# Kernel tuning notes

Hardware: AMD Instinct MI355X
Metric: run time of the kernel (lower is better)

## Reference

```python
import jax, jax.numpy as jnp
import numpy as np

B, T, C = 4, 4096, 1024
DIM_K, DIM_V = 64, 64


def setup_inputs() -> dict:
    key = jax.random.key(0)
    k1, k2, k3, k4, k5, k6 = jax.random.split(key, 6)
    q_embs = jax.random.normal(k1, (B, T, C), dtype=jnp.float32)
    k_embs = jax.random.normal(k2, (B, T, C), dtype=jnp.float32)
    v_embs = jax.random.normal(k3, (B, T, C), dtype=jnp.float32)
    # nn.Linear(C, dim) weights have shape (dim, C); y = x @ W.T
    s = 1.0 / np.sqrt(C)
    w_q = jax.random.uniform(k4, (DIM_K, C), jnp.float32, -s, s)
    w_k = jax.random.uniform(k5, (DIM_K, C), jnp.float32, -s, s)
    w_v = jax.random.uniform(k6, (DIM_V, C), jnp.float32, -s, s)
    return {"q_embs": q_embs, "k_embs": k_embs, "v_embs": v_embs,
            "w_q": w_q, "w_k": w_k, "w_v": w_v}


def reference(q_embs, k_embs, v_embs, w_q, w_k, w_v):
    Bv, Tv, Cv = v_embs.shape
    q = jnp.einsum('btc,kc->btk', q_embs, w_q)  # [B,T,dim_k]
    k = jnp.einsum('btc,kc->btk', k_embs, w_k)  # [B,T,dim_k]
    v = jnp.einsum('btc,vc->btv', v_embs, w_v)  # [B,T,dim_v]
    # NOTE: original scales by C**-0.5 (embedding dim), not dim_k**-0.5
    scores = jnp.einsum('bqk,bsk->bqs', q, k) * (Cv ** -0.5)  # [B,T,T]
    causal = jnp.tril(jnp.ones((Tv, Tv), dtype=bool))
    scores = jnp.where(causal, scores, -jnp.inf)
    wei = jax.nn.softmax(scores, axis=-1)
    return jnp.einsum('bqs,bsv->bqv', wei, v)  # [B,T,dim_v]
```

## Files before the change

### kernel.cpp

```cpp
#include <hip/hip_runtime.h>

#define TSEQ 4096
#define CDIM 1024
#define DHEAD 64

typedef __bf16 bf16x8 __attribute__((ext_vector_type(8)));
typedef float f32x4 __attribute__((ext_vector_type(4)));

__global__ __launch_bounds__(256) void wconv_kernel(
    const float* __restrict__ wq, const float* __restrict__ wk,
    const float* __restrict__ wv, __bf16* __restrict__ Wb)
{
  const int t = blockIdx.x * 256 + threadIdx.x;
  const int idx = t * 8;
  const int pid = idx >> 16;
  const float* __restrict__ src = (pid == 0) ? wq : ((pid == 1) ? wk : wv);
  const int off = idx & 65535;
  f32x4 a = *(const f32x4*)(src + off);
  f32x4 b = *(const f32x4*)(src + off + 4);
  ushort4 lo, hi;
  lo.x = __builtin_bit_cast(unsigned short, (__bf16)a[0]);
  lo.y = __builtin_bit_cast(unsigned short, (__bf16)a[1]);
  lo.z = __builtin_bit_cast(unsigned short, (__bf16)a[2]);
  lo.w = __builtin_bit_cast(unsigned short, (__bf16)a[3]);
  hi.x = __builtin_bit_cast(unsigned short, (__bf16)b[0]);
  hi.y = __builtin_bit_cast(unsigned short, (__bf16)b[1]);
  hi.z = __builtin_bit_cast(unsigned short, (__bf16)b[2]);
  hi.w = __builtin_bit_cast(unsigned short, (__bf16)b[3]);
  *(ushort4*)(Wb + idx) = lo;
  *(ushort4*)(Wb + idx + 4) = hi;
}

#define PKCH 64
#define PNCH (CDIM / PKCH)

__global__ __launch_bounds__(256) void proj_kernel(
    const float* __restrict__ qe, const float* __restrict__ ke,
    const float* __restrict__ ve, const __bf16* __restrict__ Wb,
    __bf16* __restrict__ Qo, __bf16* __restrict__ Ko, __bf16* __restrict__ Vto)
{
  __shared__ __align__(16) float Abuf[2][64 * PKCH];

  const int pid = blockIdx.y;
  const float* __restrict__ emb = (pid == 0) ? qe : ((pid == 1) ? ke : ve);
  const __bf16* __restrict__ W = Wb + (size_t)pid * DHEAD * CDIM;

  const int wave = threadIdx.x >> 6;
  const int lane = threadIdx.x & 63;
  const int g = lane >> 4, c = lane & 15;
  const int bm0 = blockIdx.x * 64;
  const int m0 = bm0 + wave * 16;

  size_t gsrc[4];
  int lofs[4];
#pragma unroll
  for (int j = 0; j < 4; ++j) {
    const int row = (wave * 4 + j) * 4 + (lane >> 4);
    const int colb = ((lane & 15) << 4) ^ ((row & 7) << 4);
    gsrc[j] = (size_t)(bm0 + row) * CDIM + (colb >> 2);
    lofs[j] = (wave * 4 + j) * 256;
  }

  const int arow = wave * 16 + c;
  const int aswz = (arow & 7) << 4;
  int ra0[2], ra1[2];
#pragma unroll
  for (int ks = 0; ks < 2; ++ks) {
    const int ncol = ks * 128 + g * 32;
    ra0[ks] = arow * 256 + ((ncol) ^ aswz);
    ra1[ks] = arow * 256 + ((ncol + 16) ^ aswz);
  }

  f32x4 acc[4];
#pragma unroll
  for (int n = 0; n < 4; ++n) acc[n] = (f32x4){0.f, 0.f, 0.f, 0.f};

  auto stage = [&](int buf, int ch) {
    const float* __restrict__ eb = emb + (size_t)ch * PKCH;
    float* lb = &Abuf[buf][0];
#pragma unroll
    for (int j = 0; j < 4; ++j) {
      __builtin_amdgcn_global_load_lds(
          (const __attribute__((address_space(1))) void*)(uintptr_t)(eb + gsrc[j]),
          (__attribute__((address_space(3))) void*)(unsigned)(uintptr_t)(lb + lofs[j]),
          16, 0, 0);
    }
  };

  stage(0, 0);
  __syncthreads();

  for (int ch = 0; ch < PNCH; ++ch) {
    if (ch + 1 < PNCH) stage((ch + 1) & 1, ch + 1);
    const char* base = (const char*)&Abuf[ch & 1][0];
    const __bf16* __restrict__ wp = W + (size_t)ch * PKCH + g * 8;
#pragma unroll
    for (int ks = 0; ks < 2; ++ks) {
      f32x4 lo = *(const f32x4*)(base + ra0[ks]);
      f32x4 hi = *(const f32x4*)(base + ra1[ks]);
      bf16x8 af;
      af[0] = (__bf16)lo[0];
      af[1] = (__bf16)lo[1];
      af[2] = (__bf16)lo[2];
      af[3] = (__bf16)lo[3];
      af[4] = (__bf16)hi[0];
      af[5] = (__bf16)hi[1];
      af[6] = (__bf16)hi[2];
      af[7] = (__bf16)hi[3];
#pragma unroll
      for (int n = 0; n < 4; ++n) {
        bf16x8 wf = *(const bf16x8*)(wp + (size_t)(n * 16 + c) * CDIM + ks * 32);
        acc[n] = __builtin_amdgcn_mfma_f32_16x16x32_bf16(af, wf, acc[n], 0, 0, 0);
      }
    }
    __syncthreads();
  }

  if (pid < 2) {
    __bf16* __restrict__ dst = (pid == 0) ? Qo : Ko;
#pragma unroll
    for (int n = 0; n < 4; ++n)
#pragma unroll
      for (int r = 0; r < 4; ++r)
        dst[(size_t)(m0 + g * 4 + r) * DHEAD + n * 16 + c] = (__bf16)acc[n][r];
  } else {
    const int t0 = m0 + g * 4;
    const int bb = t0 >> 12;
    const int tl = t0 & (TSEQ - 1);
#pragma unroll
    for (int n = 0; n < 4; ++n) {
      const int v = n * 16 + c;
      ushort4 pk;
      pk.x = __builtin_bit_cast(unsigned short, (__bf16)acc[n][0]);
      pk.y = __builtin_bit_cast(unsigned short, (__bf16)acc[n][1]);
      pk.z = __builtin_bit_cast(unsigned short, (__bf16)acc[n][2]);
      pk.w = __builtin_bit_cast(unsigned short, (__bf16)acc[n][3]);
      *(ushort4*)(Vto + ((size_t)bb * DHEAD + v) * TSEQ + tl) = pk;
    }
  }
}

#define NWAVE 8

__global__ __launch_bounds__(512) void attn_kernel(
    const __bf16* __restrict__ Q, const __bf16* __restrict__ K,
    const __bf16* __restrict__ Vt, float* __restrict__ out)
{
  __shared__ __bf16 Plds[NWAVE][16][72];
  __shared__ float Om[NWAVE][16][65];
  __shared__ float La[NWAVE][16];

  const int b = blockIdx.y;
  const int tile = (int)gridDim.x - 1 - (int)blockIdx.x;
  const int q0 = tile * 16;
  const int wave = threadIdx.x >> 6;
  const int lane = threadIdx.x & 63;
  const int g = lane >> 4, c = lane & 15;

  const __bf16* Qb = Q + (size_t)b * TSEQ * DHEAD;
  const __bf16* Kb = K + (size_t)b * TSEQ * DHEAD;
  const __bf16* Vb = Vt + (size_t)b * DHEAD * TSEQ;

  bf16x8 aq0 = *(const bf16x8*)(Qb + (size_t)(q0 + c) * DHEAD + g * 8);
  bf16x8 aq1 = *(const bf16x8*)(Qb + (size_t)(q0 + c) * DHEAD + 32 + g * 8);

  bf16x8 ones;
#pragma unroll
  for (int j = 0; j < 8; ++j) ones[j] = (__bf16)1.0f;

  f32x4 o[4];
#pragma unroll
  for (int n = 0; n < 4; ++n) o[n] = (f32x4){0.f, 0.f, 0.f, 0.f};
  f32x4 lacc = (f32x4){0.f, 0.f, 0.f, 0.f};

  const float kScale = 0.04508422f;
  const int nt = (q0 + 16 + 63) >> 6;

  for (int st = wave; st < nt; st += 2 * NWAVE) {
    const int s0A = st * 64;
    const int stB = st + NWAVE;
    const bool hasB = stB < nt;
    const int s0B = stB * 64;

    bf16x8 ka0[4], ka1[4], kb0[4], kb1[4];
#pragma unroll
    for (int n = 0; n < 4; ++n) {
      const __bf16* kp = Kb + (size_t)(s0A + n * 16 + c) * DHEAD + g * 8;
      ka0[n] = *(const bf16x8*)(kp);
      ka1[n] = *(const bf16x8*)(kp + 32);
    }
    if (hasB) {
#pragma unroll
      for (int n = 0; n < 4; ++n) {
        const __bf16* kp = Kb + (size_t)(s0B + n * 16 + c) * DHEAD + g * 8;
        kb0[n] = *(const bf16x8*)(kp);
        kb1[n] = *(const bf16x8*)(kp + 32);
      }
    }

    f32x4 sA[4];
#pragma unroll
    for (int n = 0; n < 4; ++n) {
      f32x4 z = (f32x4){0.f, 0.f, 0.f, 0.f};
      z = __builtin_amdgcn_mfma_f32_16x16x32_bf16(aq0, ka0[n], z, 0, 0, 0);
      sA[n] = __builtin_amdgcn_mfma_f32_16x16x32_bf16(aq1, ka1[n], z, 0, 0, 0);
    }
    bf16x8 va0[4], va1[4];
#pragma unroll
    for (int n = 0; n < 4; ++n) {
      const __bf16* vp = Vb + (size_t)(n * 16 + c) * TSEQ + s0A + g * 8;
      va0[n] = *(const bf16x8*)(vp);
      va1[n] = *(const bf16x8*)(vp + 32);
    }
#pragma unroll
    for (int n = 0; n < 4; ++n) {
      const int sidx = s0A + n * 16 + c;
#pragma unroll
      for (int r = 0; r < 4; ++r) {
        const int qidx = q0 + g * 4 + r;
        float p = (sidx <= qidx) ? __builtin_amdgcn_exp2f(sA[n][r] * kScale) : 0.f;
        Plds[wave][g * 4 + r][n * 16 + c] = (__bf16)p;
      }
    }

    f32x4 sB[4];
    bf16x8 vb0[4], vb1[4];
    if (hasB) {
#pragma unroll
      for (int n = 0; n < 4; ++n) {
        f32x4 z = (f32x4){0.f, 0.f, 0.f, 0.f};
        z = __builtin_amdgcn_mfma_f32_16x16x32_bf16(aq0, kb0[n], z, 0, 0, 0);
        sB[n] = __builtin_amdgcn_mfma_f32_16x16x32_bf16(aq1, kb1[n], z, 0, 0, 0);
      }
#pragma unroll
      for (int n = 0; n < 4; ++n) {
        const __bf16* vp = Vb + (size_t)(n * 16 + c) * TSEQ + s0B + g * 8;
        vb0[n] = *(const bf16x8*)(vp);
        vb1[n] = *(const bf16x8*)(vp + 32);
      }
    }

    bf16x8 p0A = *(const bf16x8*)(&Plds[wave][c][g * 8]);
    bf16x8 p1A = *(const bf16x8*)(&Plds[wave][c][32 + g * 8]);
    lacc = __builtin_amdgcn_mfma_f32_16x16x32_bf16(p0A, ones, lacc, 0, 0, 0);
    lacc = __builtin_amdgcn_mfma_f32_16x16x32_bf16(p1A, ones, lacc, 0, 0, 0);

    if (hasB) {
#pragma unroll
      for (int n = 0; n < 4; ++n) {
        const int sidx = s0B + n * 16 + c;
#pragma unroll
        for (int r = 0; r < 4; ++r) {
          const int qidx = q0 + g * 4 + r;
          float p = (sidx <= qidx) ? __builtin_amdgcn_exp2f(sB[n][r] * kScale) : 0.f;
          Plds[wave][g * 4 + r][n * 16 + c] = (__bf16)p;
        }
      }
    }

#pragma unroll
    for (int n = 0; n < 4; ++n) {
      o[n] = __builtin_amdgcn_mfma_f32_16x16x32_bf16(p0A, va0[n], o[n], 0, 0, 0);
      o[n] = __builtin_amdgcn_mfma_f32_16x16x32_bf16(p1A, va1[n], o[n], 0, 0, 0);
    }

    if (hasB) {
      bf16x8 p0B = *(const bf16x8*)(&Plds[wave][c][g * 8]);
      bf16x8 p1B = *(const bf16x8*)(&Plds[wave][c][32 + g * 8]);
      lacc = __builtin_amdgcn_mfma_f32_16x16x32_bf16(p0B, ones, lacc, 0, 0, 0);
      lacc = __builtin_amdgcn_mfma_f32_16x16x32_bf16(p1B, ones, lacc, 0, 0, 0);
#pragma unroll
      for (int n = 0; n < 4; ++n) {
        o[n] = __builtin_amdgcn_mfma_f32_16x16x32_bf16(p0B, vb0[n], o[n], 0, 0, 0);
        o[n] = __builtin_amdgcn_mfma_f32_16x16x32_bf16(p1B, vb1[n], o[n], 0, 0, 0);
      }
    }
  }

#pragma unroll
  for (int n = 0; n < 4; ++n)
#pragma unroll
    for (int r = 0; r < 4; ++r)
      Om[wave][g * 4 + r][n * 16 + c] = o[n][r];
  if (c == 0) {
#pragma unroll
    for (int r = 0; r < 4; ++r) La[wave][g * 4 + r] = lacc[r];
  }
  __syncthreads();

  const int tid = threadIdx.x;
  const int q = tid >> 5;
  const int c2 = (tid & 31) * 2;
  float l = 0.f;
#pragma unroll
  for (int w = 0; w < NWAVE; ++w) l += La[w][q];
  float s0 = 0.f, s1 = 0.f;
#pragma unroll
  for (int w = 0; w < NWAVE; ++w) {
    s0 += Om[w][q][c2];
    s1 += Om[w][q][c2 + 1];
  }
  const float inv = 1.0f / l;
  float2 r;
  r.x = s0 * inv;
  r.y = s1 * inv;
  *(float2*)(out + ((size_t)b * TSEQ + q0 + q) * DHEAD + c2) = r;
}

extern "C" void kernel_launch(void* const* d_in, const int* in_sizes, int n_in,
                              void* d_out, int out_size, void* d_ws, size_t ws_size,
                              hipStream_t stream) {
  const float* qe = (const float*)d_in[0];
  const float* ke = (const float*)d_in[1];
  const float* ve = (const float*)d_in[2];
  const float* wq = (const float*)d_in[3];
  const float* wk = (const float*)d_in[4];
  const float* wv = (const float*)d_in[5];

  __bf16* Qw  = (__bf16*)d_ws;
  __bf16* Kw  = Qw + (size_t)4 * TSEQ * DHEAD;
  __bf16* Vtw = Kw + (size_t)4 * TSEQ * DHEAD;
  __bf16* Wb  = Vtw + (size_t)4 * TSEQ * DHEAD;

  wconv_kernel<<<dim3(96), dim3(256), 0, stream>>>(wq, wk, wv, Wb);

  dim3 g1(4 * TSEQ / 64, 3), b1(256);
  proj_kernel<<<g1, b1, 0, stream>>>(qe, ke, ve, Wb, Qw, Kw, Vtw);

  dim3 g2(TSEQ / 16, 4), b2(512);
  attn_kernel<<<g2, b2, 0, stream>>>(Qw, Kw, Vtw, (float*)d_out);
}
```

Measured before the change: 279.8 us.

## Split projection K dimension across waves with 16-row blocks and LDS reduction

The projection kernel now gives each block 16 rows instead of 64. It loads each row's full 1024-float embedding into LDS in one shot rather than double-buffering 64-wide chunks. Each of the four waves covers a quarter of the K dimension, and the partial accumulators are summed through LDS before vectorized bf16 stores of Q/K and transposed V. The grid grows fourfold to raise memory-level parallelism on this bandwidth-bound stage. In exchange, each block uses 64KB of LDS, which limits blocks per CU, adds a cross-wave reduction, and drops the load/compute pipelining.

```diff
diff --git a/kernel.cpp b/kernel.cpp
--- a/kernel.cpp
+++ b/kernel.cpp
@@ -31,112 +31,102 @@
   *(ushort4*)(Wb + idx + 4) = hi;
 }
 
-#define PKCH 64
-#define PNCH (CDIM / PKCH)
-
 __global__ __launch_bounds__(256) void proj_kernel(
     const float* __restrict__ qe, const float* __restrict__ ke,
     const float* __restrict__ ve, const __bf16* __restrict__ Wb,
     __bf16* __restrict__ Qo, __bf16* __restrict__ Ko, __bf16* __restrict__ Vto)
 {
-  __shared__ __align__(16) float Abuf[2][64 * PKCH];
+  __shared__ __align__(16) float Alds[16 * 1024];
 
   const int pid = blockIdx.y;
   const float* __restrict__ emb = (pid == 0) ? qe : ((pid == 1) ? ke : ve);
   const __bf16* __restrict__ W = Wb + (size_t)pid * DHEAD * CDIM;
 
-  const int wave = threadIdx.x >> 6;
+  const int wav = threadIdx.x >> 6;
   const int lane = threadIdx.x & 63;
   const int g = lane >> 4, c = lane & 15;
-  const int bm0 = blockIdx.x * 64;
-  const int m0 = bm0 + wave * 16;
-
-  size_t gsrc[4];
-  int lofs[4];
-#pragma unroll
-  for (int j = 0; j < 4; ++j) {
-    const int row = (wave * 4 + j) * 4 + (lane >> 4);
-    const int colb = ((lane & 15) << 4) ^ ((row & 7) << 4);
-    gsrc[j] = (size_t)(bm0 + row) * CDIM + (colb >> 2);
-    lofs[j] = (wave * 4 + j) * 256;
-  }
-
-  const int arow = wave * 16 + c;
-  const int aswz = (arow & 7) << 4;
-  int ra0[2], ra1[2];
-#pragma unroll
-  for (int ks = 0; ks < 2; ++ks) {
-    const int ncol = ks * 128 + g * 32;
-    ra0[ks] = arow * 256 + ((ncol) ^ aswz);
-    ra1[ks] = arow * 256 + ((ncol + 16) ^ aswz);
-  }
+  const int m0 = blockIdx.x * 16;
+
+#pragma unroll
+  for (int r = 0; r < 16; ++r) {
+    const float* src = emb + (size_t)(m0 + r) * CDIM + wav * 256 + ((lane ^ (r & 7)) << 2);
+    float* dst = Alds + r * 1024 + wav * 256;
+    __builtin_amdgcn_global_load_lds(
+        (const __attribute__((address_space(1))) void*)(uintptr_t)src,
+        (__attribute__((address_space(3))) void*)(unsigned)(uintptr_t)dst,
+        16, 0, 0);
+  }
+  asm volatile("s_waitcnt vmcnt(0)" ::: "memory");
 
   f32x4 acc[4];
 #pragma unroll
   for (int n = 0; n < 4; ++n) acc[n] = (f32x4){0.f, 0.f, 0.f, 0.f};
 
-  auto stage = [&](int buf, int ch) {
-    const float* __restrict__ eb = emb + (size_t)ch * PKCH;
-    float* lb = &Abuf[buf][0];
-#pragma unroll
-    for (int j = 0; j < 4; ++j) {
-      __builtin_amdgcn_global_load_lds(
-          (const __attribute__((address_space(1))) void*)(uintptr_t)(eb + gsrc[j]),
-          (__attribute__((address_space(3))) void*)(unsigned)(uintptr_t)(lb + lofs[j]),
-          16, 0, 0);
-    }
-  };
-
-  stage(0, 0);
+  const int cswz = c & 7;
+  const __bf16* __restrict__ wbase = W + (size_t)c * CDIM + wav * 256 + g * 8;
+#pragma unroll
+  for (int ks = 0; ks < 8; ++ks) {
+    const float* ab = Alds + c * 1024 + wav * 256 + ks * 32;
+    f32x4 lo = *(const f32x4*)(ab + (((g * 2 + 0) ^ cswz) << 2));
+    f32x4 hi = *(const f32x4*)(ab + (((g * 2 + 1) ^ cswz) << 2));
+    bf16x8 af;
+    af[0] = (__bf16)lo[0];
+    af[1] = (__bf16)lo[1];
+    af[2] = (__bf16)lo[2];
+    af[3] = (__bf16)lo[3];
+    af[4] = (__bf16)hi[0];
+    af[5] = (__bf16)hi[1];
+    af[6] = (__bf16)hi[2];
+    af[7] = (__bf16)hi[3];
+#pragma unroll
+    for (int n = 0; n < 4; ++n) {
+      bf16x8 wf = *(const bf16x8*)(wbase + (size_t)n * 16 * CDIM + ks * 32);
+      acc[n] = __builtin_amdgcn_mfma_f32_16x16x32_bf16(af, wf, acc[n], 0, 0, 0);
+    }
+  }
+
   __syncthreads();
-
-  for (int ch = 0; ch < PNCH; ++ch) {
-    if (ch + 1 < PNCH) stage((ch + 1) & 1, ch + 1);
-    const char* base = (const char*)&Abuf[ch & 1][0];
-    const __bf16* __restrict__ wp = W + (size_t)ch * PKCH + g * 8;
-#pragma unroll
-    for (int ks = 0; ks < 2; ++ks) {
-      f32x4 lo = *(const f32x4*)(base + ra0[ks]);
-      f32x4 hi = *(const f32x4*)(base + ra1[ks]);
-      bf16x8 af;
-      af[0] = (__bf16)lo[0];
-      af[1] = (__bf16)lo[1];
-      af[2] = (__bf16)lo[2];
-      af[3] = (__bf16)lo[3];
-      af[4] = (__bf16)hi[0];
-      af[5] = (__bf16)hi[1];
-      af[6] = (__bf16)hi[2];
-      af[7] = (__bf16)hi[3];
-#pragma unroll
-      for (int n = 0; n < 4; ++n) {
-        bf16x8 wf = *(const bf16x8*)(wp + (size_t)(n * 16 + c) * CDIM + ks * 32);
-        acc[n] = __builtin_amdgcn_mfma_f32_16x16x32_bf16(af, wf, acc[n], 0, 0, 0);
-      }
-    }
-    __syncthreads();
-  }
-
+  float* Ored = Alds;
+#pragma unroll
+  for (int n = 0; n < 4; ++n)
+#pragma unroll
+    for (int r = 0; r < 4; ++r)
+      Ored[wav * 1152 + (g * 4 + r) * 72 + n * 16 + c] = acc[n][r];
+  __syncthreads();
+
+  const int t = threadIdx.x;
   if (pid < 2) {
     __bf16* __restrict__ dst = (pid == 0) ? Qo : Ko;
-#pragma unroll
-    for (int n = 0; n < 4; ++n)
-#pragma unroll
-      for (int r = 0; r < 4; ++r)
-        dst[(size_t)(m0 + g * 4 + r) * DHEAD + n * 16 + c] = (__bf16)acc[n][r];
+    const int row = t >> 4, c4 = (t & 15) * 4;
+    f32x4 s = (f32x4){0.f, 0.f, 0.f, 0.f};
+#pragma unroll
+    for (int w2 = 0; w2 < 4; ++w2) {
+      f32x4 p = *(const f32x4*)&Ored[w2 * 1152 + row * 72 + c4];
+      s[0] += p[0]; s[1] += p[1]; s[2] += p[2]; s[3] += p[3];
+    }
+    ushort4 pk;
+    pk.x = __builtin_bit_cast(unsigned short, (__bf16)s[0]);
+    pk.y = __builtin_bit_cast(unsigned short, (__bf16)s[1]);
+    pk.z = __builtin_bit_cast(unsigned short, (__bf16)s[2]);
+    pk.w = __builtin_bit_cast(unsigned short, (__bf16)s[3]);
+    *(ushort4*)(dst + (size_t)(m0 + row) * DHEAD + c4) = pk;
   } else {
-    const int t0 = m0 + g * 4;
-    const int bb = t0 >> 12;
-    const int tl = t0 & (TSEQ - 1);
-#pragma unroll
-    for (int n = 0; n < 4; ++n) {
-      const int v = n * 16 + c;
-      ushort4 pk;
-      pk.x = __builtin_bit_cast(unsigned short, (__bf16)acc[n][0]);
-      pk.y = __builtin_bit_cast(unsigned short, (__bf16)acc[n][1]);
-      pk.z = __builtin_bit_cast(unsigned short, (__bf16)acc[n][2]);
-      pk.w = __builtin_bit_cast(unsigned short, (__bf16)acc[n][3]);
-      *(ushort4*)(Vto + ((size_t)bb * DHEAD + v) * TSEQ + tl) = pk;
-    }
+    const int v = t >> 2, tq = (t & 3) * 4;
+    const int bb = m0 >> 12;
+    const int tl = m0 & (TSEQ - 1);
+    float s[4];
+#pragma unroll
+    for (int j = 0; j < 4; ++j) {
+      s[j] = 0.f;
+#pragma unroll
+      for (int w2 = 0; w2 < 4; ++w2) s[j] += Ored[w2 * 1152 + (tq + j) * 72 + v];
+    }
+    ushort4 pk;
+    pk.x = __builtin_bit_cast(unsigned short, (__bf16)s[0]);
+    pk.y = __builtin_bit_cast(unsigned short, (__bf16)s[1]);
+    pk.z = __builtin_bit_cast(unsigned short, (__bf16)s[2]);
+    pk.w = __builtin_bit_cast(unsigned short, (__bf16)s[3]);
+    *(ushort4*)(Vto + ((size_t)bb * DHEAD + v) * TSEQ + tl + tq) = pk;
   }
 }
 
@@ -324,7 +314,7 @@
 
   wconv_kernel<<<dim3(96), dim3(256), 0, stream>>>(wq, wk, wv, Wb);
 
-  dim3 g1(4 * TSEQ / 64, 3), b1(256);
+  dim3 g1(4 * TSEQ / 16, 3), b1(256);
   proj_kernel<<<g1, b1, 0, stream>>>(qe, ke, ve, Wb, Qw, Kw, Vtw);
 
   dim3 g2(TSEQ / 16, 4), b2(512);
```

Measured after the change: 303.7 us. 1.09x slower.
